# Optimization experiments

Hardware: AMD Instinct MI355X
Metric: run time of the kernel (lower is better)

Reference implementation:

```python
import jax, jax.numpy as jnp
import numpy as np

NH = 16  # num_heads


def _ln(x, eps=1e-6):
    m = x.mean(-1, keepdims=True)
    v = ((x - m) ** 2).mean(-1, keepdims=True)
    return (x - m) * jax.lax.rsqrt(v + eps)


def _mod(z, sh, sc):
    return z * (1 + sc[:, None, :]) + sh[:, None, :]


def _attn(q, k, v, out_w, out_b, nh=NH):
    B, S, E = q.shape
    hd = E // nh
    q = q.reshape(B, S, nh, hd)
    k = k.reshape(B, -1, nh, hd)
    v = v.reshape(B, -1, nh, hd)
    s = jnp.einsum('bqhd,bkhd->bhqk', q, k) / float(np.sqrt(hd))
    a = jax.nn.softmax(s, axis=-1)
    o = jnp.einsum('bhqk,bkhd->bqhd', a, v).reshape(B, S, E)
    return o @ out_w.T + out_b


def setup_inputs() -> dict:
    key = jax.random.key(0)
    ks = jax.random.split(key, 40)
    E, L, Ne, I, p, C, clip, Kd = 1024, 2, 8, 4096, 2, 4, 768, 1536
    N = (64 // p) ** 2
    n = lambda k, shape, s=0.02: (jax.random.normal(k, shape, jnp.float32) * s)
    inp = {
        'x': jax.random.normal(ks[0], (2, C, 64, 64), jnp.float32),
        't': jax.random.uniform(ks[1], (2,), jnp.float32) * 1000.0,
        'clip_vec': jax.random.normal(ks[2], (2, clip), jnp.float32),
        'qwen_context': jax.random.normal(ks[3], (2, 256, Kd), jnp.float32),
        'conv_w': n(ks[4], (E, C, p, p)),
        'conv_b': n(ks[5], (E,)),
        'pos_embed': n(ks[6], (1, N, E)),
        'tmlp_w1': n(ks[7], (256, 256)), 'tmlp_b1': n(ks[8], (256,)),
        'tmlp_w2': n(ks[9], (256, 256)), 'tmlp_b2': n(ks[10], (256,)),
        'cond_w': n(ks[11], (E, 256 + clip)), 'cond_b': n(ks[12], (E,)),
        'ada_w': n(ks[13], (L, 9 * E, E)), 'ada_b': n(ks[14], (L, 9 * E)),
        'sa_in_w': n(ks[15], (L, 3 * E, E)), 'sa_in_b': n(ks[16], (L, 3 * E)),
        'sa_out_w': n(ks[17], (L, E, E)), 'sa_out_b': n(ks[18], (L, E)),
        'ca_q_w': n(ks[19], (L, E, E)), 'ca_k_w': n(ks[20], (L, E, Kd)),
        'ca_v_w': n(ks[21], (L, E, Kd)), 'ca_in_b': n(ks[22], (L, 3 * E)),
        'ca_out_w': n(ks[23], (L, E, E)), 'ca_out_b': n(ks[24], (L, E)),
        'gate_w': n(ks[25], (L, Ne, E)), 'gate_b': n(ks[26], (L, Ne)),
        'e_w1': n(ks[27], (L, Ne, I, E)), 'e_b1': n(ks[28], (L, Ne, I)),
        'e_w2': n(ks[29], (L, Ne, E, I)), 'e_b2': n(ks[30], (L, Ne, E)),
        'fin_w': n(ks[31], (p * p * C, E)), 'fin_b': n(ks[32], (p * p * C,)),
    }
    return inp


def reference(x, t, clip_vec, qwen_context, conv_w, conv_b, pos_embed,
              tmlp_w1, tmlp_b1, tmlp_w2, tmlp_b2, cond_w, cond_b,
              ada_w, ada_b, sa_in_w, sa_in_b, sa_out_w, sa_out_b,
              ca_q_w, ca_k_w, ca_v_w, ca_in_b, ca_out_w, ca_out_b,
              gate_w, gate_b, e_w1, e_b1, e_w2, e_b2, fin_w, fin_b):
    B, C, H, W = x.shape
    E, p = conv_w.shape[0], conv_w.shape[-1]
    h, w = H // p, W // p
    # patch-embed conv (kernel==stride) as unfold + matmul
    patches = x.reshape(B, C, h, p, w, p).transpose(0, 2, 4, 1, 3, 5).reshape(B, h * w, C * p * p)
    xt = patches @ conv_w.reshape(E, -1).T + conv_b + pos_embed
    # sinusoidal timestep embedding (dim 256)
    half = 128
    freqs = jnp.exp(jnp.arange(half, dtype=jnp.float32) * (-np.log(10000.0) / (half - 1)))
    te = t[:, None] * freqs[None, :]
    te = jnp.concatenate([jnp.sin(te), jnp.cos(te)], -1)
    te = jax.nn.silu(te @ tmlp_w1.T + tmlp_b1) @ tmlp_w2.T + tmlp_b2
    c = jnp.concatenate([te, clip_vec], -1) @ cond_w.T + cond_b  # [B,E]
    depth = ada_w.shape[0]
    for i in range(depth):
        pr = jax.nn.silu(c) @ ada_w[i].T + ada_b[i]
        sh_sa, sc_sa, g_sa, sh_ca, sc_ca, g_ca, sh_m, sc_m, g_m = jnp.split(pr, 9, axis=1)
        # self-attention
        xn = _mod(_ln(xt), sh_sa, sc_sa)
        qkv = xn @ sa_in_w[i].T + sa_in_b[i]
        q, k, v = jnp.split(qkv, 3, axis=-1)
        xt = xt + g_sa[:, None, :] * _attn(q, k, v, sa_out_w[i], sa_out_b[i])
        # cross-attention with separate q/k/v projections
        xn = _mod(_ln(xt), sh_ca, sc_ca)
        q = xn @ ca_q_w[i].T + ca_in_b[i, :E]
        k = qwen_context @ ca_k_w[i].T + ca_in_b[i, E:2 * E]
        v = qwen_context @ ca_v_w[i].T + ca_in_b[i, 2 * E:]
        xt = xt + g_ca[:, None, :] * _attn(q, k, v, ca_out_w[i], ca_out_b[i])
        # top-2 sparse MoE (dense-combine formulation: zero weight for unrouted experts)
        xn = _mod(_ln(xt), sh_m, sc_m)
        probs = jax.nn.softmax(xn @ gate_w[i].T + gate_b[i], axis=-1)
        tw, ti = jax.lax.top_k(probs, 2)
        tw = tw / (tw.sum(-1, keepdims=True) + 1e-6)
        wd = (jax.nn.one_hot(ti, probs.shape[-1], dtype=xn.dtype) * tw[..., None]).sum(-2)  # [B,S,Ne]
        hid = jax.nn.gelu(jnp.einsum('bsd,eid->bsei', xn, e_w1[i]) + e_b1[i], approximate=True)
        y = jnp.einsum('bsei,eoi->bseo', hid, e_w2[i]) + e_b2[i]
        moe = jnp.einsum('bseo,bse->bso', y, wd)
        xt = xt + g_m[:, None, :] * moe
    # final layer + unpatchify (nhwpqc->nchpwq)
    xt = _ln(xt) @ fin_w.T + fin_b
    out = xt.reshape(B, h, w, p, p, C).transpose(0, 5, 1, 3, 2, 4).reshape(B, C, h * p, w * p)
    return out
```

## Files before the change

### kernel.cpp

```cpp
#include <hip/hip_runtime.h>
#include <hip/hip_bf16.h>

#define B_ 2
#define S_ 1024
#define E_ 1024
#define NHEAD 16
#define NE 8
#define II 4096
#define KD 1536
#define CLIP_ 768
#define TOK (B_*S_)

typedef short bf16x8 __attribute__((ext_vector_type(8)));
typedef float f32x4 __attribute__((ext_vector_type(4)));

__device__ __forceinline__ float siluf(float x){ return x/(1.f+expf(-x)); }
__device__ __forceinline__ float geluf(float x){
    float x3 = x*x*x;
    return 0.5f*x*(1.f+tanhf(0.7978845608028654f*(x+0.044715f*x3)));
}
__device__ __forceinline__ unsigned short h16(float x){
    union { __hip_bfloat16 b; unsigned short u; } c;
    c.b = __float2bfloat16(x);
    return c.u;
}
__device__ __forceinline__ unsigned pk2(float a, float b){
    return (unsigned)h16(a) | ((unsigned)h16(b)<<16);
}
__device__ __forceinline__ void sp(float a, unsigned& hb, unsigned& lb){
    unsigned short h = h16(a);
    float r = a - __uint_as_float(((unsigned)h)<<16);
    hb = h; lb = h16(r);
}

union U8 { unsigned u[4]; bf16x8 v; uint4 q; };

__global__ void k_patch_embed(const float* __restrict__ x, const float* __restrict__ cw,
                              const float* __restrict__ cb, const float* __restrict__ pos,
                              float* __restrict__ xt){
    int token = blockIdx.x;
    int b = token >> 10, n = token & 1023;
    int hh = n >> 5, ww = n & 31;
    __shared__ float patch[16];
    int tid = threadIdx.x;
    if (tid < 16){
        int c = tid >> 2, py = (tid >> 1) & 1, px = tid & 1;
        patch[tid] = x[(((size_t)b*4 + c)*64 + hh*2+py)*64 + ww*2+px];
    }
    __syncthreads();
    for (int e = tid; e < E_; e += 256){
        float acc = cb[e];
        #pragma unroll
        for (int j=0;j<16;j++) acc += patch[j]*cw[e*16+j];
        xt[(size_t)token*E_ + e] = acc + pos[(size_t)n*E_ + e];
    }
}

__global__ void k_time_cond(const float* __restrict__ t, const float* __restrict__ clip,
                            const float* __restrict__ w1, const float* __restrict__ b1,
                            const float* __restrict__ w2, const float* __restrict__ b2,
                            const float* __restrict__ cw, const float* __restrict__ cbias,
                            float* __restrict__ silu_c){
    int b = blockIdx.x, tid = threadIdx.x;
    __shared__ float te[256], h1[256], te2[256];
    if (tid < 128){
        float f = expf((float)tid * (-9.210340371976184f/127.f));
        float a = t[b]*f;
        te[tid]     = sinf(a);
        te[tid+128] = cosf(a);
    }
    __syncthreads();
    {
        float acc = b1[tid];
        const float* wr = w1 + (size_t)tid*256;
        for (int k=0;k<256;k++) acc += te[k]*wr[k];
        h1[tid] = siluf(acc);
    }
    __syncthreads();
    {
        float acc = b2[tid];
        const float* wr = w2 + (size_t)tid*256;
        for (int k=0;k<256;k++) acc += h1[k]*wr[k];
        te2[tid] = acc;
    }
    __syncthreads();
    const float* cl = clip + (size_t)b*CLIP_;
    for (int e = tid; e < E_; e += 256){
        float acc = cbias[e];
        const float* wr = cw + (size_t)e*1024;
        for (int k=0;k<256;k++)  acc += te2[k]*wr[k];
        for (int k=0;k<CLIP_;k++) acc += cl[k]*wr[256+k];
        silu_c[b*E_+e] = siluf(acc);
    }
}

__global__ void k_ada2(const float* __restrict__ sic, const float* __restrict__ aw,
                       const float* __restrict__ ab, float* __restrict__ pr){
    int row = blockIdx.x*4 + (threadIdx.x>>6);
    int lane = threadIdx.x & 63;
    const float* w = aw + (size_t)row*1024;
    float a0 = 0.f, a1 = 0.f;
    #pragma unroll
    for (int it=0; it<4; it++){
        int k = it*256 + lane*4;
        float4 wv = *(const float4*)(w+k);
        float4 x0 = *(const float4*)(sic+k);
        float4 x1 = *(const float4*)(sic+1024+k);
        a0 += wv.x*x0.x + wv.y*x0.y + wv.z*x0.z + wv.w*x0.w;
        a1 += wv.x*x1.x + wv.y*x1.y + wv.z*x1.z + wv.w*x1.w;
    }
    #pragma unroll
    for (int off=32; off; off>>=1){ a0 += __shfl_down(a0,off); a1 += __shfl_down(a1,off); }
    if (lane==0){
        float bb = ab[row];
        pr[row] = a0 + bb;
        pr[9*E_ + row] = a1 + bb;
    }
}

__global__ void k_ln_mod(const float* __restrict__ src, float* __restrict__ dst32,
                         unsigned short* __restrict__ dsth, unsigned short* __restrict__ dstl,
                         const float* __restrict__ pr, int shc, int scc){
    int token = blockIdx.x, tid = threadIdx.x;
    int b = token >> 10;
    const float* row = src + (size_t)token*E_;
    float4 v = *(const float4*)(row + tid*4);
    float s = v.x+v.y+v.z+v.w;
    float ss = v.x*v.x+v.y*v.y+v.z*v.z+v.w*v.w;
    #pragma unroll
    for (int off=32; off; off>>=1){ s += __shfl_down(s,off); ss += __shfl_down(ss,off); }
    __shared__ float rs_[4], rss_[4];
    int wid = tid >> 6;
    if ((tid&63)==0){ rs_[wid]=s; rss_[wid]=ss; }
    __syncthreads();
    s  = rs_[0]+rs_[1]+rs_[2]+rs_[3];
    ss = rss_[0]+rss_[1]+rss_[2]+rss_[3];
    float mean = s*(1.f/1024.f);
    float rstd = rsqrtf(ss*(1.f/1024.f) - mean*mean + 1e-6f);
    const float* shv = pr + b*9*E_ + shc*E_;
    const float* scv = pr + b*9*E_ + scc*E_;
    int e = tid*4;
    float o[4];
    float4 sc4 = *(const float4*)(scv+e);
    float4 sh4 = *(const float4*)(shv+e);
    o[0] = (v.x-mean)*rstd*(1.f+sc4.x) + sh4.x;
    o[1] = (v.y-mean)*rstd*(1.f+sc4.y) + sh4.y;
    o[2] = (v.z-mean)*rstd*(1.f+sc4.z) + sh4.z;
    o[3] = (v.w-mean)*rstd*(1.f+sc4.w) + sh4.w;
    if (dst32) *(float4*)(dst32 + (size_t)token*E_ + e) = make_float4(o[0],o[1],o[2],o[3]);
    unsigned hu[2], lu[2];
    {
        unsigned h0,l0,h1,l1;
        sp(o[0],h0,l0); sp(o[1],h1,l1);
        hu[0]=h0|(h1<<16); lu[0]=l0|(l1<<16);
        sp(o[2],h0,l0); sp(o[3],h1,l1);
        hu[1]=h0|(h1<<16); lu[1]=l0|(l1<<16);
    }
    *(uint2*)(dsth + (size_t)token*E_ + e) = make_uint2(hu[0],hu[1]);
    *(uint2*)(dstl + (size_t)token*E_ + e) = make_uint2(lu[0],lu[1]);
}

__global__ void k_split4(const float* __restrict__ src, unsigned short* __restrict__ hp,
                         unsigned short* __restrict__ lp, int n4){
    int i = blockIdx.x*256 + threadIdx.x;
    if (i >= n4) return;
    float4 v = *(const float4*)(src + i*4);
    unsigned h0,l0,h1,l1,h2,l2,h3,l3;
    sp(v.x,h0,l0); sp(v.y,h1,l1); sp(v.z,h2,l2); sp(v.w,h3,l3);
    *(uint2*)(hp + i*4) = make_uint2(h0|(h1<<16), h2|(h3<<16));
    *(uint2*)(lp + i*4) = make_uint2(l0|(l1<<16), l2|(l3<<16));
}

template<int MOE, int EPI, int GATHER, int TERMS>
__global__ __launch_bounds__(256) void k_mm(
    const unsigned short* __restrict__ Ahpp, const unsigned short* __restrict__ Alpp, int lda,
    const float* __restrict__ Wp, int ldw,
    const float* __restrict__ biasp, int bstride,
    void* __restrict__ Cp, void* __restrict__ Cp2, int ldc,
    int M, int N, int K,
    const float* __restrict__ pr, int gch,
    const int* __restrict__ cnt, const int* __restrict__ offs,
    const int* __restrict__ list)
{
    constexpr int NPL = (TERMS==3) ? 2 : 1;
    int e  = MOE ? blockIdx.z : 0;
    int Mm = MOE ? cnt[e] : M;
    int bm = blockIdx.y*128;
    if (MOE && bm >= Mm) return;
    int o0 = MOE ? offs[e] : 0;
    int bn = blockIdx.x*128;
    const float* W = Wp + (size_t)e*N*ldw;
    const float* bias = biasp + (size_t)e*bstride;

    __shared__ __align__(16) unsigned short As_[2][NPL][128*40];
    __shared__ __align__(16) unsigned short Bs_[2][NPL][128*40];

    int tid = threadIdx.x;
    int lane = tid & 63, wid = tid >> 6;
    int wm = wid >> 1, wn = wid & 1;

    int srow = tid >> 1, shalf = tid & 1;
    int sbase = srow*40 + shalf*16;
    int amr = bm + srow; if (amr >= Mm) amr = Mm - 1;
    int arow;
    if (MOE) arow = GATHER ? list[o0 + amr] : (o0 + amr);
    else     arow = amr;
    const unsigned short* Ahp = Ahpp + (size_t)arow*lda + shalf*16;
    const unsigned short* Alp = (TERMS==3) ? (Alpp + (size_t)arow*lda + shalf*16) : nullptr;
    const float* Bf = W + (size_t)(bn + srow)*ldw + shalf*16;

    float fB[16];
    uint4 aH0, aH1, aL0, aL1;

    auto LOAD = [&](int k0){
        aH0 = *(const uint4*)(Ahp+k0);
        aH1 = *(const uint4*)(Ahp+k0+8);
        if (TERMS==3){
            aL0 = *(const uint4*)(Alp+k0);
            aL1 = *(const uint4*)(Alp+k0+8);
        }
        *(float4*)(fB+0)  = *(const float4*)(Bf+k0+0);
        *(float4*)(fB+4)  = *(const float4*)(Bf+k0+4);
        *(float4*)(fB+8)  = *(const float4*)(Bf+k0+8);
        *(float4*)(fB+12) = *(const float4*)(Bf+k0+12);
    };
    auto STAGE = [&](int buf){
        *(uint4*)&As_[buf][0][sbase]   = aH0;
        *(uint4*)&As_[buf][0][sbase+8] = aH1;
        if (TERMS==3){
            *(uint4*)&As_[buf][NPL-1][sbase]   = aL0;
            *(uint4*)&As_[buf][NPL-1][sbase+8] = aL1;
        }
        if (TERMS==3){
            unsigned hb2[8], lb2[8];
            #pragma unroll
            for (int i=0;i<8;i++){
                unsigned h0,l0,h1,l1;
                sp(fB[2*i],h0,l0); sp(fB[2*i+1],h1,l1);
                hb2[i]=h0|(h1<<16); lb2[i]=l0|(l1<<16);
            }
            *(uint4*)&Bs_[buf][0][sbase]   = make_uint4(hb2[0],hb2[1],hb2[2],hb2[3]);
            *(uint4*)&Bs_[buf][0][sbase+8] = make_uint4(hb2[4],hb2[5],hb2[6],hb2[7]);
            *(uint4*)&Bs_[buf][NPL-1][sbase]   = make_uint4(lb2[0],lb2[1],lb2[2],lb2[3]);
            *(uint4*)&Bs_[buf][NPL-1][sbase+8] = make_uint4(lb2[4],lb2[5],lb2[6],lb2[7]);
        } else {
            unsigned hb2[8];
            #pragma unroll
            for (int i=0;i<8;i++) hb2[i] = pk2(fB[2*i],fB[2*i+1]);
            *(uint4*)&Bs_[buf][0][sbase]   = make_uint4(hb2[0],hb2[1],hb2[2],hb2[3]);
            *(uint4*)&Bs_[buf][0][sbase+8] = make_uint4(hb2[4],hb2[5],hb2[6],hb2[7]);
        }
    };

    f32x4 acc[4][4];
    #pragma unroll
    for (int m=0;m<4;m++)
        #pragma unroll
        for (int n=0;n<4;n++) acc[m][n] = (f32x4){0.f,0.f,0.f,0.f};

    int fr = lane & 15, fko = (lane>>4)*8, fr4 = (lane>>4)*4;

    LOAD(0);
    STAGE(0);
    __syncthreads();
    int cur = 0;
    for (int k0=0; k0<K; k0+=32){
        bool nxt = (k0+32) < K;
        if (nxt) LOAD(k0+32);
        bf16x8 ah[4], bh[4], al[4], bl[4];
        #pragma unroll
        for (int m=0;m<4;m++){
            int off = (wm*64 + m*16 + fr)*40 + fko;
            ah[m] = *(const bf16x8*)&As_[cur][0][off];
            if (TERMS==3) al[m] = *(const bf16x8*)&As_[cur][NPL-1][off];
        }
        #pragma unroll
        for (int n=0;n<4;n++){
            int off = (wn*64 + n*16 + fr)*40 + fko;
            bh[n] = *(const bf16x8*)&Bs_[cur][0][off];
            if (TERMS==3) bl[n] = *(const bf16x8*)&Bs_[cur][NPL-1][off];
        }
        #pragma unroll
        for (int m=0;m<4;m++)
            #pragma unroll
            for (int n=0;n<4;n++){
                acc[m][n] = __builtin_amdgcn_mfma_f32_16x16x32_bf16(ah[m], bh[n], acc[m][n], 0, 0, 0);
                if (TERMS==3){
                    acc[m][n] = __builtin_amdgcn_mfma_f32_16x16x32_bf16(ah[m], bl[n], acc[m][n], 0, 0, 0);
                    acc[m][n] = __builtin_amdgcn_mfma_f32_16x16x32_bf16(al[m], bh[n], acc[m][n], 0, 0, 0);
                }
            }
        if (nxt) STAGE(cur^1);
        __syncthreads();
        cur ^= 1;
    }

    #pragma unroll
    for (int m=0;m<4;m++){
        #pragma unroll
        for (int j=0;j<4;j++){
            int row = bm + wm*64 + m*16 + fr4 + j;
            if (row >= Mm) continue;
            #pragma unroll
            for (int n=0;n<4;n++){
                int col = bn + wn*64 + n*16 + fr;
                float v = acc[m][n][j] + bias[col];
                if (EPI==0){
                    ((float*)Cp)[(size_t)row*ldc + col] = v;
                } else if (EPI==1){
                    int bb = row >> 10;
                    ((float*)Cp)[(size_t)row*ldc + col] += pr[bb*9*E_ + gch*E_ + col] * v;
                } else if (EPI==2){
                    if (TERMS==3){
                        unsigned hb, lb; sp(geluf(v), hb, lb);
                        ((unsigned short*)Cp )[(size_t)(o0+row)*ldc + col] = (unsigned short)hb;
                        ((unsigned short*)Cp2)[(size_t)(o0+row)*ldc + col] = (unsigned short)lb;
                    } else {
                        ((unsigned short*)Cp )[(size_t)(o0+row)*ldc + col] = h16(geluf(v));
                    }
                } else {
                    ((float*)Cp)[(size_t)(o0+row)*ldc + col] = v;
                }
            }
        }
    }
}

__global__ __launch_bounds__(256) void k_attn_m(
    const float* __restrict__ qp, int qstride,
    const float* __restrict__ kp, const float* __restrict__ vp, int kvstride,
    unsigned short* __restrict__ oph, unsigned short* __restrict__ opl,
    int ostride, int Sq, int Sk, float scale)
{
    __shared__ __align__(16) unsigned short Kh[64*72];
    __shared__ __align__(16) unsigned short Kl[64*72];
    __shared__ __align__(16) unsigned V_i[64*70];
    __shared__ __align__(16) unsigned short P_[4][2][16*72];

    int tid = threadIdx.x, lane = tid & 63, wid = tid >> 6;
    int g = lane >> 4, fr = lane & 15;
    int h = blockIdx.y, b = blockIdx.z;
    int qbase = blockIdx.x*64;

    bf16x8 qh[2], ql[2];
    {
        const float* qr = qp + (size_t)(b*Sq + qbase + wid*16 + fr)*qstride + h*64;
        #pragma unroll
        for (int ds=0; ds<2; ds++){
            float f[8];
            *(float4*)(f+0) = *(const float4*)(qr + ds*32 + g*8);
            *(float4*)(f+4) = *(const float4*)(qr + ds*32 + g*8 + 4);
            U8 uh, ul;
            #pragma unroll
            for (int i=0;i<4;i++){
                unsigned h0,l0,h1,l1;
                sp(f[2*i]*scale, h0,l0); sp(f[2*i+1]*scale, h1,l1);
                uh.u[i] = h0|(h1<<16); ul.u[i] = l0|(l1<<16);
            }
            qh[ds] = uh.v; ql[ds] = ul.v;
        }
    }

    float m_run = -1e30f, l_run = 0.f;
    f32x4 oacc[4];
    #pragma unroll
    for (int dt=0;dt<4;dt++) oacc[dt] = (f32x4){0.f,0.f,0.f,0.f};

    unsigned short* PhW = &P_[wid][0][0];
    unsigned short* PlW = &P_[wid][1][0];

    for (int kt0 = 0; kt0 < Sk; kt0 += 64){
        __syncthreads();
        {
            int srow = tid >> 2, d0 = (tid & 3) << 4;
            size_t grow = (size_t)(b*Sk + kt0 + srow)*kvstride + h*64 + d0;
            {
                const float* srcp = kp + grow;
                float f[16];
                *(float4*)(f+0)  = *(const float4*)(srcp+0);
                *(float4*)(f+4)  = *(const float4*)(srcp+4);
                *(float4*)(f+8)  = *(const float4*)(srcp+8);
                *(float4*)(f+12) = *(const float4*)(srcp+12);
                U8 uh0, uh1, ul0, ul1;
                #pragma unroll
                for (int i=0;i<4;i++){
                    unsigned a0,b0,a1,b1;
                    sp(f[2*i],a0,b0); sp(f[2*i+1],a1,b1);
                    uh0.u[i] = a0|(a1<<16); ul0.u[i] = b0|(b1<<16);
                }
                #pragma unroll
                for (int i=0;i<4;i++){
                    unsigned a0,b0,a1,b1;
                    sp(f[8+2*i],a0,b0); sp(f[8+2*i+1],a1,b1);
                    uh1.u[i] = a0|(a1<<16); ul1.u[i] = b0|(b1<<16);
                }
                int base = srow*72 + d0;
                *(uint4*)&Kh[base]     = uh0.q;
                *(uint4*)&Kh[base + 8] = uh1.q;
                *(uint4*)&Kl[base]     = ul0.q;
                *(uint4*)&Kl[base + 8] = ul1.q;
            }
            {
                const float* srcp = vp + grow;
                float f[16];
                *(float4*)(f+0)  = *(const float4*)(srcp+0);
                *(float4*)(f+4)  = *(const float4*)(srcp+4);
                *(float4*)(f+8)  = *(const float4*)(srcp+8);
                *(float4*)(f+12) = *(const float4*)(srcp+12);
                int base = srow*70 + d0;
                #pragma unroll
                for (int i4=0;i4<4;i4++){
                    U8 u;
                    #pragma unroll
                    for (int i=0;i<4;i++){
                        unsigned hb, lb; sp(f[4*i4+i], hb, lb);
                        u.u[i] = hb | (lb<<16);
                    }
                    *(uint2*)&V_i[base + i4*4]     = make_uint2(u.u[0], u.u[1]);
                    *(uint2*)&V_i[base + i4*4 + 2] = make_uint2(u.u[2], u.u[3]);
                }
            }
        }
        __syncthreads();

        f32x4 st[4];
        #pragma unroll
        for (int kt=0;kt<4;kt++) st[kt] = (f32x4){0.f,0.f,0.f,0.f};
        #pragma unroll
        for (int ds=0; ds<2; ds++){
            #pragma unroll
            for (int kt=0;kt<4;kt++){
                int row = kt*16 + fr;
                int so = row*72 + ds*32 + g*8;
                bf16x8 kh  = *(const bf16x8*)&Kh[so];
                bf16x8 klo = *(const bf16x8*)&Kl[so];
                st[kt] = __builtin_amdgcn_mfma_f32_16x16x32_bf16(kh, qh[ds], st[kt], 0,0,0);
                st[kt] = __builtin_amdgcn_mfma_f32_16x16x32_bf16(kh, ql[ds], st[kt], 0,0,0);
                st[kt] = __builtin_amdgcn_mfma_f32_16x16x32_bf16(klo, qh[ds], st[kt], 0,0,0);
            }
        }

        float pmax = -1e30f;
        #pragma unroll
        for (int kt=0;kt<4;kt++)
            #pragma unroll
            for (int r=0;r<4;r++) pmax = fmaxf(pmax, st[kt][r]);
        pmax = fmaxf(pmax, __shfl_xor(pmax, 16));
        pmax = fmaxf(pmax, __shfl_xor(pmax, 32));
        float mnew = fmaxf(m_run, pmax);
        float p[4][4]; float psum = 0.f;
        #pragma unroll
        for (int kt=0;kt<4;kt++)
            #pragma unroll
            for (int r=0;r<4;r++){ float pv = expf(st[kt][r] - mnew); p[kt][r] = pv; psum += pv; }
        psum += __shfl_xor(psum, 16);
        psum += __shfl_xor(psum, 32);
        float corr = expf(m_run - mnew);
        l_run = l_run*corr + psum;
        m_run = mnew;
        #pragma unroll
        for (int j=0;j<4;j++){
            float cj = __shfl(corr, g*4 + j);
            #pragma unroll
            for (int dt=0;dt<4;dt++) oacc[dt][j] *= cj;
        }

        #pragma unroll
        for (int kt=0;kt<4;kt++){
            unsigned h0,l0,h1,l1,h2,l2,h3,l3;
            sp(p[kt][0],h0,l0); sp(p[kt][1],h1,l1);
            sp(p[kt][2],h2,l2); sp(p[kt][3],h3,l3);
            int base = fr*72 + kt*16 + g*4;
            *(unsigned*)&PhW[base]     = h0|(h1<<16);
            *(unsigned*)&PhW[base + 2] = h2|(h3<<16);
            *(unsigned*)&PlW[base]     = l0|(l1<<16);
            *(unsigned*)&PlW[base + 2] = l2|(l3<<16);
        }

        #pragma unroll
        for (int ks=0; ks<2; ks++){
            int pso = fr*72 + ks*32 + g*8;
            bf16x8 ph = *(const bf16x8*)&PhW[pso];
            bf16x8 pl = *(const bf16x8*)&PlW[pso];
            #pragma unroll
            for (int dt=0; dt<4; dt++){
                unsigned w[8];
                #pragma unroll
                for (int j=0;j<8;j++){
                    int row = ks*32 + g*8 + j;
                    w[j] = V_i[row*70 + dt*16 + fr];
                }
                U8 vh, vl;
                #pragma unroll
                for (int i=0;i<4;i++){
                    vh.u[i] = (w[2*i] & 0xffffu) | (w[2*i+1] << 16);
                    vl.u[i] = (w[2*i] >> 16)     | (w[2*i+1] & 0xffff0000u);
                }
                oacc[dt] = __builtin_amdgcn_mfma_f32_16x16x32_bf16(ph, vh.v, oacc[dt], 0,0,0);
                oacc[dt] = __builtin_amdgcn_mfma_f32_16x16x32_bf16(ph, vl.v, oacc[dt], 0,0,0);
                oacc[dt] = __builtin_amdgcn_mfma_f32_16x16x32_bf16(pl, vh.v, oacc[dt], 0,0,0);
            }
        }
    }

    float linv = 1.f / l_run;
    #pragma unroll
    for (int j=0;j<4;j++){
        float lj = __shfl(linv, g*4 + j);
        int row = qbase + wid*16 + g*4 + j;
        size_t obase = (size_t)(b*Sq + row)*ostride + h*64;
        #pragma unroll
        for (int dt=0;dt<4;dt++){
            unsigned hb, lb; sp(oacc[dt][j]*lj, hb, lb);
            oph[obase + dt*16 + fr] = (unsigned short)hb;
            opl[obase + dt*16 + fr] = (unsigned short)lb;
        }
    }
}

__global__ void k_route(const float* __restrict__ xn, const float* __restrict__ gw,
                        const float* __restrict__ gb, int* __restrict__ i01,
                        float* __restrict__ w01, int* __restrict__ cnt){
    int token = blockIdx.x, lane = threadIdx.x;
    const float* row = xn + (size_t)token*E_;
    float part[8] = {0,0,0,0,0,0,0,0};
    for (int k = lane; k < E_; k += 64){
        float xv = row[k];
        #pragma unroll
        for (int e=0;e<8;e++) part[e] += xv*gw[e*E_+k];
    }
    #pragma unroll
    for (int e=0;e<8;e++){
        #pragma unroll
        for (int off=32; off; off>>=1) part[e] += __shfl_down(part[e], off);
    }
    if (lane==0){
        float lg[8]; float mx = -1e30f;
        #pragma unroll
        for (int e=0;e<8;e++){ lg[e] = part[e]+gb[e]; if (lg[e]>mx) mx = lg[e]; }
        float sum = 0.f;
        #pragma unroll
        for (int e=0;e<8;e++){ lg[e] = expf(lg[e]-mx); sum += lg[e]; }
        int a0 = 0;
        #pragma unroll
        for (int e=1;e<8;e++) if (lg[e] > lg[a0]) a0 = e;
        int a1 = (a0==0)?1:0;
        #pragma unroll
        for (int e=0;e<8;e++) if (e!=a0 && lg[e] > lg[a1]) a1 = e;
        float p0 = lg[a0]/sum, p1 = lg[a1]/sum;
        float inv = 1.f/(p0+p1+1e-6f);
        i01[token*2+0]=a0; i01[token*2+1]=a1;
        w01[token*2+0]=p0*inv; w01[token*2+1]=p1*inv;
        atomicAdd(&cnt[a0],1); atomicAdd(&cnt[a1],1);
    }
}

__global__ void k_scan(const int* __restrict__ cnt, int* __restrict__ offs, int* __restrict__ curs){
    if (threadIdx.x==0 && blockIdx.x==0){
        int o = 0;
        for (int e=0;e<8;e++){ offs[e]=o; curs[e]=o; o += cnt[e]; }
    }
}

__global__ void k_place(const int* __restrict__ i01,
                        int* __restrict__ curs, int* __restrict__ list,
                        int* __restrict__ t2s){
    int t = blockIdx.x*256 + threadIdx.x;
    if (t >= TOK) return;
    #pragma unroll
    for (int s=0;s<2;s++){
        int e = i01[t*2+s];
        int p = atomicAdd(&curs[e],1);
        list[p] = t;
        t2s[t*2+s] = p;
    }
}

__global__ void k_moe_combine2(float* __restrict__ xt, const float* __restrict__ yslot,
                               const int* __restrict__ t2s, const float* __restrict__ w01,
                               const float* __restrict__ pr){
    int idx = blockIdx.x*256 + threadIdx.x;
    int token = idx >> 10, n = idx & 1023;
    int b = token >> 10;
    int s0 = t2s[token*2], s1 = t2s[token*2+1];
    float mo = w01[token*2]*yslot[(size_t)s0*E_+n] + w01[token*2+1]*yslot[(size_t)s1*E_+n];
    xt[idx] += pr[b*9*E_ + 8*E_ + n]*mo;
}

__global__ void k_final(const float* __restrict__ xt, const float* __restrict__ fw,
                        const float* __restrict__ fb, float* __restrict__ out){
    int token = blockIdx.x, tid = threadIdx.x;
    int b = token >> 10, n = token & 1023, hh = n >> 5, ww = n & 31;
    const float* row = xt + (size_t)token*E_;
    float4 v = *(const float4*)(row + tid*4);
    float s = v.x+v.y+v.z+v.w;
    float ss = v.x*v.x+v.y*v.y+v.z*v.z+v.w*v.w;
    #pragma unroll
    for (int off=32; off; off>>=1){ s += __shfl_down(s,off); ss += __shfl_down(ss,off); }
    __shared__ float rs_[4], rss_[4];
    int wid = tid >> 6;
    if ((tid&63)==0){ rs_[wid]=s; rss_[wid]=ss; }
    __syncthreads();
    s  = rs_[0]+rs_[1]+rs_[2]+rs_[3];
    ss = rss_[0]+rss_[1]+rss_[2]+rss_[3];
    float mean = s*(1.f/1024.f);
    float rstd = rsqrtf(ss*(1.f/1024.f) - mean*mean + 1e-6f);
    __shared__ float xl[1024];
    int e = tid*4;
    xl[e+0]=(v.x-mean)*rstd; xl[e+1]=(v.y-mean)*rstd;
    xl[e+2]=(v.z-mean)*rstd; xl[e+3]=(v.w-mean)*rstd;
    __syncthreads();
    int o = tid & 15, seg = tid >> 4;
    float part = 0.f;
    const float* wr = fw + (size_t)o*E_ + seg*64;
    const float* xr = xl + seg*64;
    #pragma unroll 8
    for (int j=0;j<64;j++) part += xr[j]*wr[j];
    __shared__ float ps[16][17];
    ps[seg][o] = part;
    __syncthreads();
    if (tid < 16){
        float acc = fb[tid];
        #pragma unroll
        for (int s2=0;s2<16;s2++) acc += ps[s2][tid];
        int py = tid>>3, px = (tid>>2)&1, ch = tid&3;
        out[(((size_t)b*4+ch)*64 + hh*2+py)*64 + ww*2+px] = acc;
    }
}

extern "C" void kernel_launch(void* const* d_in, const int* in_sizes, int n_in,
                              void* d_out, int out_size, void* d_ws, size_t ws_size,
                              hipStream_t stream){
    const float* x        = (const float*)d_in[0];
    const float* t        = (const float*)d_in[1];
    const float* clip     = (const float*)d_in[2];
    const float* qwen     = (const float*)d_in[3];
    const float* conv_w   = (const float*)d_in[4];
    const float* conv_b   = (const float*)d_in[5];
    const float* pos      = (const float*)d_in[6];
    const float* tw1      = (const float*)d_in[7];
    const float* tb1      = (const float*)d_in[8];
    const float* tw2      = (const float*)d_in[9];
    const float* tb2      = (const float*)d_in[10];
    const float* cond_w   = (const float*)d_in[11];
    const float* cond_b   = (const float*)d_in[12];
    const float* ada_w    = (const float*)d_in[13];
    const float* ada_b    = (const float*)d_in[14];
    const float* sa_in_w  = (const float*)d_in[15];
    const float* sa_in_b  = (const float*)d_in[16];
    const float* sa_out_w = (const float*)d_in[17];
    const float* sa_out_b = (const float*)d_in[18];
    const float* ca_q_w   = (const float*)d_in[19];
    const float* ca_k_w   = (const float*)d_in[20];
    const float* ca_v_w   = (const float*)d_in[21];
    const float* ca_in_b  = (const float*)d_in[22];
    const float* ca_out_w = (const float*)d_in[23];
    const float* ca_out_b = (const float*)d_in[24];
    const float* gate_w   = (const float*)d_in[25];
    const float* gate_b   = (const float*)d_in[26];
    const float* e_w1     = (const float*)d_in[27];
    const float* e_b1     = (const float*)d_in[28];
    const float* e_w2     = (const float*)d_in[29];
    const float* e_b2     = (const float*)d_in[30];
    const float* fin_w    = (const float*)d_in[31];
    const float* fin_b    = (const float*)d_in[32];

    float* ws    = (float*)d_ws;
    float* xt    = ws;
    float* xn    = ws + 2097152;
    float* qkv   = ws + 4194304;
    float* yslot = qkv;
    unsigned short* xnh = (unsigned short*)(ws + 10485760);
    unsigned short* xnl = (unsigned short*)(ws + 11534336);
    unsigned short* obh = (unsigned short*)(ws + 12582912);
    unsigned short* obl = (unsigned short*)(ws + 13631488);
    unsigned short* hidh = (unsigned short*)(ws + 14680064);
    unsigned short* hidl = (unsigned short*)(ws + 23068672);
    unsigned short* qwh = (unsigned short*)(ws + 31457280);
    unsigned short* qwl = (unsigned short*)(ws + 31981568);
    float* kbuf  = ws + 32505856;
    float* vbuf  = ws + 33030144;
    float* pr    = ws + 33554432;
    float* sic   = ws + 33572864;
    float* w01   = ws + 33574912;
    int*   i01   = (int*)(ws + 33579008);
    int*   t2s   = (int*)(ws + 33583104);
    int*   list  = (int*)(ws + 33587200);
    int*   cnt   = (int*)(ws + 33591296);
    int*   offs  = cnt + 8;
    int*   curs  = cnt + 16;

    k_patch_embed<<<TOK,256,0,stream>>>(x, conv_w, conv_b, pos, xt);
    k_time_cond<<<B_,256,0,stream>>>(t, clip, tw1, tb1, tw2, tb2, cond_w, cond_b, sic);
    k_split4<<<(B_*256*KD/4+255)/256,256,0,stream>>>(qwen, qwh, qwl, B_*256*KD/4);

    for (int i=0;i<2;i++){
        k_ada2<<<2304,256,0,stream>>>(sic, ada_w + (size_t)i*9*E_*E_,
                                      ada_b + (size_t)i*9*E_, pr);
        k_ln_mod<<<TOK,256,0,stream>>>(xt, nullptr, xnh, xnl, pr, 0, 1);
        k_mm<0,0,0,3><<<dim3(24,16),256,0,stream>>>(
            xnh, xnl, E_, sa_in_w + (size_t)i*3*E_*E_, E_, sa_in_b + (size_t)i*3*E_, 0,
            qkv, nullptr, 3*E_, TOK, 3*E_, E_, nullptr, 0, nullptr, nullptr, nullptr);
        k_attn_m<<<dim3(16,NHEAD,B_),256,0,stream>>>(qkv, 3*E_, qkv+E_, qkv+2*E_, 3*E_,
                                                     obh, obl, E_, S_, S_, 0.125f);
        k_mm<0,1,0,3><<<dim3(8,16),256,0,stream>>>(
            obh, obl, E_, sa_out_w + (size_t)i*E_*E_, E_, sa_out_b + (size_t)i*E_, 0,
            xt, nullptr, E_, TOK, E_, E_, pr, 2, nullptr, nullptr, nullptr);
        k_ln_mod<<<TOK,256,0,stream>>>(xt, nullptr, xnh, xnl, pr, 3, 4);
        k_mm<0,0,0,3><<<dim3(8,16),256,0,stream>>>(
            xnh, xnl, E_, ca_q_w + (size_t)i*E_*E_, E_, ca_in_b + (size_t)i*3*E_, 0,
            qkv, nullptr, E_, TOK, E_, E_, nullptr, 0, nullptr, nullptr, nullptr);
        k_mm<0,0,0,3><<<dim3(8,4),256,0,stream>>>(
            qwh, qwl, KD, ca_k_w + (size_t)i*E_*KD, KD, ca_in_b + (size_t)i*3*E_ + E_, 0,
            kbuf, nullptr, E_, B_*256, E_, KD, nullptr, 0, nullptr, nullptr, nullptr);
        k_mm<0,0,0,3><<<dim3(8,4),256,0,stream>>>(
            qwh, qwl, KD, ca_v_w + (size_t)i*E_*KD, KD, ca_in_b + (size_t)i*3*E_ + 2*E_, 0,
            vbuf, nullptr, E_, B_*256, E_, KD, nullptr, 0, nullptr, nullptr, nullptr);
        k_attn_m<<<dim3(16,NHEAD,B_),256,0,stream>>>(qkv, E_, kbuf, vbuf, E_,
                                                     obh, obl, E_, S_, 256, 0.125f);
        k_mm<0,1,0,3><<<dim3(8,16),256,0,stream>>>(
            obh, obl, E_, ca_out_w + (size_t)i*E_*E_, E_, ca_out_b + (size_t)i*E_, 0,
            xt, nullptr, E_, TOK, E_, E_, pr, 5, nullptr, nullptr, nullptr);
        k_ln_mod<<<TOK,256,0,stream>>>(xt, xn, xnh, xnl, pr, 6, 7);
        hipMemsetAsync(cnt, 0, 8*sizeof(int), stream);
        k_route<<<TOK,64,0,stream>>>(xn, gate_w + (size_t)i*NE*E_, gate_b + (size_t)i*NE,
                                     i01, w01, cnt);
        k_scan<<<1,64,0,stream>>>(cnt, offs, curs);
        k_place<<<TOK/256,256,0,stream>>>(i01, curs, list, t2s);
        if (i==0){
            k_mm<1,2,1,3><<<dim3(32,32,NE),256,0,stream>>>(
                xnh, xnl, E_, e_w1 + (size_t)i*NE*II*E_, E_, e_b1 + (size_t)i*NE*II, II,
                hidh, hidl, II, 0, II, E_, nullptr, 0, cnt, offs, list);
            k_mm<1,3,0,3><<<dim3(8,32,NE),256,0,stream>>>(
                hidh, hidl, II, e_w2 + (size_t)i*NE*E_*II, II, e_b2 + (size_t)i*NE*E_, E_,
                yslot, nullptr, E_, 0, E_, II, nullptr, 0, cnt, offs, list);
        } else {
            k_mm<1,2,1,1><<<dim3(32,32,NE),256,0,stream>>>(
                xnh, nullptr, E_, e_w1 + (size_t)i*NE*II*E_, E_, e_b1 + (size_t)i*NE*II, II,
                hidh, nullptr, II, 0, II, E_, nullptr, 0, cnt, offs, list);
            k_mm<1,3,0,1><<<dim3(8,32,NE),256,0,stream>>>(
                hidh, nullptr, II, e_w2 + (size_t)i*NE*E_*II, II, e_b2 + (size_t)i*NE*E_, E_,
                yslot, nullptr, E_, 0, E_, II, nullptr, 0, cnt, offs, list);
        }
        k_moe_combine2<<<TOK*E_/256,256,0,stream>>>(xt, yslot, t2s, w01, pr);
    }
    k_final<<<TOK,256,0,stream>>>(xt, fin_w, fin_b, (float*)d_out);
}
```

Baseline: 2.154 ms.

## Load A fragments directly from global and add split-K for MoE down-projection

Removes the A-operand shared-memory staging from the shared GEMM kernel, so each wave reads its bf16 A fragments straight from global memory (gathered rows computed once per block). Adds a split-K template parameter and uses four K-chunks for the expert down-projection GEMM, accumulating partial results with float atomics into a zeroed output buffer. Split-K raises the number of blocks for the down-projection, which otherwise has few N tiles, to improve occupancy. The trade-offs are redundant global A reads across waves in every GEMM, an extra memset, atomic contention, and non-deterministic summation order.

Result: slower. 2.718 ms (+26.2%).

```diff
diff --git a/kernel.cpp b/kernel.cpp
--- a/kernel.cpp
+++ b/kernel.cpp
@@ -171,7 +171,7 @@
     *(uint2*)(lp + i*4) = make_uint2(l0|(l1<<16), l2|(l3<<16));
 }
 
-template<int MOE, int EPI, int GATHER, int TERMS>
+template<int MOE, int EPI, int GATHER, int TERMS, int SPLITK=1>
 __global__ __launch_bounds__(256) void k_mm(
     const unsigned short* __restrict__ Ahpp, const unsigned short* __restrict__ Alpp, int lda,
     const float* __restrict__ Wp, int ldw,
@@ -188,49 +188,41 @@
     int bm = blockIdx.y*128;
     if (MOE && bm >= Mm) return;
     int o0 = MOE ? offs[e] : 0;
-    int bn = blockIdx.x*128;
+    int nt = gridDim.x / SPLITK;
+    int ntile = blockIdx.x % nt;
+    int kc = blockIdx.x / nt;
+    int bn = ntile*128;
+    int kbeg = kc*(K/SPLITK), kend = kbeg + K/SPLITK;
     const float* W = Wp + (size_t)e*N*ldw;
     const float* bias = biasp + (size_t)e*bstride;
 
-    __shared__ __align__(16) unsigned short As_[2][NPL][128*40];
     __shared__ __align__(16) unsigned short Bs_[2][NPL][128*40];
 
     int tid = threadIdx.x;
     int lane = tid & 63, wid = tid >> 6;
     int wm = wid >> 1, wn = wid & 1;
+    int fr = lane & 15, fko = (lane>>4)*8, fr4 = (lane>>4)*4;
+
+    int garow[4];
+    #pragma unroll
+    for (int m=0;m<4;m++){
+        int r = bm + wm*64 + m*16 + fr;
+        if (r >= Mm) r = Mm - 1;
+        garow[m] = MOE ? (GATHER ? list[o0 + r] : (o0 + r)) : r;
+    }
 
     int srow = tid >> 1, shalf = tid & 1;
     int sbase = srow*40 + shalf*16;
-    int amr = bm + srow; if (amr >= Mm) amr = Mm - 1;
-    int arow;
-    if (MOE) arow = GATHER ? list[o0 + amr] : (o0 + amr);
-    else     arow = amr;
-    const unsigned short* Ahp = Ahpp + (size_t)arow*lda + shalf*16;
-    const unsigned short* Alp = (TERMS==3) ? (Alpp + (size_t)arow*lda + shalf*16) : nullptr;
     const float* Bf = W + (size_t)(bn + srow)*ldw + shalf*16;
 
     float fB[16];
-    uint4 aH0, aH1, aL0, aL1;
-
-    auto LOAD = [&](int k0){
-        aH0 = *(const uint4*)(Ahp+k0);
-        aH1 = *(const uint4*)(Ahp+k0+8);
-        if (TERMS==3){
-            aL0 = *(const uint4*)(Alp+k0);
-            aL1 = *(const uint4*)(Alp+k0+8);
-        }
+    auto LOADB = [&](int k0){
         *(float4*)(fB+0)  = *(const float4*)(Bf+k0+0);
         *(float4*)(fB+4)  = *(const float4*)(Bf+k0+4);
         *(float4*)(fB+8)  = *(const float4*)(Bf+k0+8);
         *(float4*)(fB+12) = *(const float4*)(Bf+k0+12);
     };
-    auto STAGE = [&](int buf){
-        *(uint4*)&As_[buf][0][sbase]   = aH0;
-        *(uint4*)&As_[buf][0][sbase+8] = aH1;
-        if (TERMS==3){
-            *(uint4*)&As_[buf][NPL-1][sbase]   = aL0;
-            *(uint4*)&As_[buf][NPL-1][sbase+8] = aL1;
-        }
+    auto STAGEB = [&](int buf){
         if (TERMS==3){
             unsigned hb2[8], lb2[8];
             #pragma unroll
@@ -258,21 +250,19 @@
         #pragma unroll
         for (int n=0;n<4;n++) acc[m][n] = (f32x4){0.f,0.f,0.f,0.f};
 
-    int fr = lane & 15, fko = (lane>>4)*8, fr4 = (lane>>4)*4;
-
-    LOAD(0);
-    STAGE(0);
+    LOADB(kbeg);
+    STAGEB(0);
     __syncthreads();
     int cur = 0;
-    for (int k0=0; k0<K; k0+=32){
-        bool nxt = (k0+32) < K;
-        if (nxt) LOAD(k0+32);
-        bf16x8 ah[4], bh[4], al[4], bl[4];
+    for (int k0=kbeg; k0<kend; k0+=32){
+        bool nxt = (k0+32) < kend;
+        if (nxt) LOADB(k0+32);
+        bf16x8 ah[4], al[4], bh[4], bl[4];
         #pragma unroll
         for (int m=0;m<4;m++){
-            int off = (wm*64 + m*16 + fr)*40 + fko;
-            ah[m] = *(const bf16x8*)&As_[cur][0][off];
-            if (TERMS==3) al[m] = *(const bf16x8*)&As_[cur][NPL-1][off];
+            size_t ao = (size_t)garow[m]*lda + k0 + fko;
+            ah[m] = *(const bf16x8*)(Ahpp + ao);
+            if (TERMS==3) al[m] = *(const bf16x8*)(Alpp + ao);
         }
         #pragma unroll
         for (int n=0;n<4;n++){
@@ -290,7 +280,7 @@
                     acc[m][n] = __builtin_amdgcn_mfma_f32_16x16x32_bf16(al[m], bh[n], acc[m][n], 0, 0, 0);
                 }
             }
-        if (nxt) STAGE(cur^1);
+        if (nxt) STAGEB(cur^1);
         __syncthreads();
         cur ^= 1;
     }
@@ -304,7 +294,8 @@
             #pragma unroll
             for (int n=0;n<4;n++){
                 int col = bn + wn*64 + n*16 + fr;
-                float v = acc[m][n][j] + bias[col];
+                float bv = (SPLITK==1 || kc==0) ? bias[col] : 0.f;
+                float v = acc[m][n][j] + bv;
                 if (EPI==0){
                     ((float*)Cp)[(size_t)row*ldc + col] = v;
                 } else if (EPI==1){
@@ -319,7 +310,10 @@
                         ((unsigned short*)Cp )[(size_t)(o0+row)*ldc + col] = h16(geluf(v));
                     }
                 } else {
-                    ((float*)Cp)[(size_t)(o0+row)*ldc + col] = v;
+                    if (SPLITK==1)
+                        ((float*)Cp)[(size_t)(o0+row)*ldc + col] = v;
+                    else
+                        atomicAdd(&((float*)Cp)[(size_t)(o0+row)*ldc + col], v);
                 }
             }
         }
@@ -727,18 +721,19 @@
                                      i01, w01, cnt);
         k_scan<<<1,64,0,stream>>>(cnt, offs, curs);
         k_place<<<TOK/256,256,0,stream>>>(i01, curs, list, t2s);
+        hipMemsetAsync(yslot, 0, (size_t)2*TOK*E_*sizeof(float), stream);
         if (i==0){
             k_mm<1,2,1,3><<<dim3(32,32,NE),256,0,stream>>>(
                 xnh, xnl, E_, e_w1 + (size_t)i*NE*II*E_, E_, e_b1 + (size_t)i*NE*II, II,
                 hidh, hidl, II, 0, II, E_, nullptr, 0, cnt, offs, list);
-            k_mm<1,3,0,3><<<dim3(8,32,NE),256,0,stream>>>(
+            k_mm<1,3,0,3,4><<<dim3(32,32,NE),256,0,stream>>>(
                 hidh, hidl, II, e_w2 + (size_t)i*NE*E_*II, II, e_b2 + (size_t)i*NE*E_, E_,
                 yslot, nullptr, E_, 0, E_, II, nullptr, 0, cnt, offs, list);
         } else {
             k_mm<1,2,1,1><<<dim3(32,32,NE),256,0,stream>>>(
                 xnh, nullptr, E_, e_w1 + (size_t)i*NE*II*E_, E_, e_b1 + (size_t)i*NE*II, II,
                 hidh, nullptr, II, 0, II, E_, nullptr, 0, cnt, offs, list);
-            k_mm<1,3,0,1><<<dim3(8,32,NE),256,0,stream>>>(
+            k_mm<1,3,0,1,4><<<dim3(32,32,NE),256,0,stream>>>(
                 hidh, nullptr, II, e_w2 + (size_t)i*NE*E_*II, II, e_b2 + (size_t)i*NE*E_, E_,
                 yslot, nullptr, E_, 0, E_, II, nullptr, 0, cnt, offs, list);
         }
```
